# Kernel tuning notes

Hardware: AMD Instinct MI355X
Metric: run time of the kernel (lower is better)

## Reference

```python
import jax, jax.numpy as jnp
import numpy as np

SEQ_LEN = 256
INPUT_DIM = 1
HIDDEN = 2048
CLASSES = 10
BATCH = 128


def setup_inputs() -> dict:
    key = jax.random.key(0)
    ks = jax.random.split(key, 6)
    x = jax.random.normal(ks[0], (BATCH, SEQ_LEN), dtype=jnp.float32)
    # Gate order along the 4H axis: g (cell candidate), i, f, o.
    Wx = jax.random.normal(ks[1], (INPUT_DIM, 4 * HIDDEN), dtype=jnp.float32) * 0.1
    Wh = jax.random.normal(ks[2], (HIDDEN, 4 * HIDDEN), dtype=jnp.float32) * (1.0 / np.sqrt(HIDDEN))
    b = jax.random.normal(ks[3], (4 * HIDDEN,), dtype=jnp.float32) * 0.1
    Wph = jax.random.normal(ks[4], (HIDDEN, CLASSES), dtype=jnp.float32) * (1.0 / np.sqrt(HIDDEN))
    bp = jax.random.normal(ks[5], (CLASSES,), dtype=jnp.float32) * 0.1
    return {"x": x, "Wx": Wx, "Wh": Wh, "b": b, "Wph": Wph, "bp": bp}


def reference(x, Wx, Wh, b, Wph, bp):
    B, T = x.shape
    H = Wh.shape[0]
    # Original loops over seq_length - 1 timesteps.
    xs = x[:, : T - 1].T[:, :, None]  # [T-1, B, 1]

    def step(carry, x_t):
        h, c = carry
        z = x_t @ Wx + h @ Wh + b  # [B, 4H] fused gate GEMM
        g = jnp.tanh(z[:, 0 * H:1 * H])
        i = jax.nn.sigmoid(z[:, 1 * H:2 * H])
        f = jax.nn.sigmoid(z[:, 2 * H:3 * H])
        o = jax.nn.sigmoid(z[:, 3 * H:4 * H])
        c = g * i + c * f
        h = jnp.tanh(c) * o
        return (h, c), None

    h0 = jnp.zeros((B, H), dtype=x.dtype)
    c0 = jnp.zeros((B, H), dtype=x.dtype)
    (h, _), _ = jax.lax.scan(step, (h0, c0), xs)
    logits = h @ Wph + bp
    return jax.nn.softmax(logits, axis=1)
```

## Files before the change

kernel.cpp:

```cpp
#include <hip/hip_runtime.h>
#include <hip/hip_bf16.h>

#define SEQ_LEN 256
#define HIDDEN  2048
#define CLASSES 10
#define BATCH   128
#define NWG     256
#define WG_THREADS 512
#define STEPS   (SEQ_LEN - 1)
#define KTILES  64
#define LDS_WH  131072
#define LDS_ALL (LDS_WH + 4096)

typedef __attribute__((ext_vector_type(8))) short  bf16x8;
typedef __attribute__((ext_vector_type(8))) unsigned short u16x8;
typedef __attribute__((ext_vector_type(4))) float  f32x4;
typedef __attribute__((ext_vector_type(4))) unsigned int u32x4;

#define WHP_OFF  0
#define HB_OFF   33554432UL
#define HF_OFF   (HB_OFF + 4UL * 524288UL)
#define BAR_OFF  (HF_OFF + 1048576UL)

__device__ __forceinline__ unsigned short f2bf(float f) {
    unsigned int u = __float_as_uint(f);
    return (unsigned short)((u + 0x7FFFu + ((u >> 16) & 1u)) >> 16);
}
__device__ __forceinline__ float sigm(float z)  { return 1.0f / (1.0f + __expf(-z)); }
__device__ __forceinline__ float tanh_f(float z){ return 2.0f / (1.0f + __expf(-2.0f * z)) - 1.0f; }

__device__ __forceinline__ unsigned int aload(const unsigned int* p) {
    return __hip_atomic_load(p, __ATOMIC_RELAXED, __HIP_MEMORY_SCOPE_AGENT);
}
__device__ __forceinline__ void astore(unsigned int* p, unsigned int v) {
    __hip_atomic_store(p, v, __ATOMIC_RELAXED, __HIP_MEMORY_SCOPE_AGENT);
}

__global__ void lstm_pack_kernel(const float* __restrict__ Wh,
                                 unsigned short* __restrict__ whp,
                                 unsigned short* __restrict__ hbufs,
                                 unsigned int* __restrict__ bar) {
    int chunk = blockIdx.x * 256 + threadIdx.x;
    int lane = chunk & 63;
    int nt   = (chunk >> 6) & 1;
    int kt   = (chunk >> 7) & 63;
    int W    = chunk >> 13;
    int q = lane >> 4, l16 = lane & 15;
    int c32  = nt * 16 + l16;
    int gate = c32 >> 3, u = c32 & 7;
    int n    = gate * 2048 + W * 8 + u;
    int k0   = kt * 32 + q * 8;
    u16x8 frag;
    #pragma unroll
    for (int j = 0; j < 8; ++j)
        frag[j] = f2bf(Wh[(size_t)(k0 + j) * 8192 + n]);
    ((u16x8*)whp)[chunk] = frag;

    if (chunk < 32768) ((u32x4*)hbufs)[chunk] = (u32x4){0, 0, 0, 0};
    if (chunk < 2048) bar[chunk] = 0u;
}

__device__ __forceinline__ void grid_barrier(unsigned int* bar, unsigned int phase,
                                             bool do_inv, int W) {
    __syncthreads();
    if (threadIdx.x < 64) {
        const int lane = threadIdx.x;
        if (lane == 0) astore(&bar[W], phase);
        if (W < 8) {
            unsigned int* sl = &bar[W * 32 + (lane & 31)];
            while (!__all((int)(aload(sl) >= phase)))
                __builtin_amdgcn_s_sleep(1);
            if (lane == 0) astore(&bar[512 + 16 * W], phase);
            if (W == 0) {
                unsigned int* dn = &bar[512 + 16 * (lane & 7)];
                while (!__all((int)(aload(dn) >= phase)))
                    __builtin_amdgcn_s_sleep(1);
                if (lane < 32) astore(&bar[1024 + 16 * lane], phase);
            }
        }
        if (lane == 0 && W != 0) {
            unsigned int* rl = &bar[1024 + 16 * (W & 31)];
            while (aload(rl) < phase)
                __builtin_amdgcn_s_sleep(1);
        }
        if (do_inv)
            __builtin_amdgcn_fence(__ATOMIC_ACQUIRE, "agent");
    }
    __syncthreads();
}

__global__ __launch_bounds__(WG_THREADS, 2) void lstm_persist(
    const float* __restrict__ x,  const float* __restrict__ Wx,
    const float* __restrict__ b,  const float* __restrict__ Wph,
    const float* __restrict__ bp, const unsigned short* __restrict__ whp,
    unsigned short* hbufs, float* hfin,
    unsigned int* bar, float* out)
{
    extern __shared__ char lds[];
    const int tid = threadIdx.x;
    const int W   = blockIdx.x;

    {
        const u32x4* src = (const u32x4*)whp + (size_t)W * 8192;
        u32x4* dst = (u32x4*)lds;
        for (int i = tid; i < 8192; i += WG_THREADS) dst[i] = src[i];
    }
    unsigned short* hstage = (unsigned short*)(lds + LDS_WH);
    __syncthreads();

    const int lane = tid & 63;
    const int wv   = tid >> 6;
    const int q    = lane >> 4;
    const int l16  = lane & 15;
    const int s    = (lane >> 3) & 1;
    const int u    = lane & 7;
    const int rowA = wv * 16 + l16;
    const int row0 = wv * 16 + q * 4;
    const int colh = W * 8 + u;

    const int n0 = ((l16) >> 3) * 2048 + W * 8 + (l16 & 7);
    const int n1 = ((16 + l16) >> 3) * 2048 + W * 8 + ((16 + l16) & 7);
    const float wx0 = Wx[n0], bb0 = b[n0];
    const float wx1 = Wx[n1], bb1 = b[n1];

    const int abase = q * 128 + rowA;

    float c_state[4] = {0.f, 0.f, 0.f, 0.f};

    for (int t = 0; t < STEPS; ++t) {
        unsigned short* hcur  = hbufs + (size_t)(t & 3) * 262144;
        unsigned short* hnext = hbufs + (size_t)((t + 1) & 3) * 262144;

        const bf16x8* hc8 = (const bf16x8*)hcur;
        const char* lp = lds + lane * 16;

        float xv[4];
        #pragma unroll
        for (int r = 0; r < 4; ++r) xv[r] = x[(row0 + r) * SEQ_LEN + t];

        f32x4 acc0 = {0.f, 0.f, 0.f, 0.f};
        f32x4 acc1 = {0.f, 0.f, 0.f, 0.f};
        bf16x8 a_cur = hc8[abase];
        #pragma unroll 8
        for (int kt = 0; kt < KTILES; ++kt) {
            bf16x8 a_nxt = (kt < KTILES - 1) ? hc8[abase + (kt + 1) * 512] : a_cur;
            bf16x8 b0 = *(const bf16x8*)(lp + (kt * 2 + 0) * 1024);
            bf16x8 b1 = *(const bf16x8*)(lp + (kt * 2 + 1) * 1024);
            acc0 = __builtin_amdgcn_mfma_f32_16x16x32_bf16(a_cur, b0, acc0, 0, 0, 0);
            acc1 = __builtin_amdgcn_mfma_f32_16x16x32_bf16(a_cur, b1, acc1, 0, 0, 0);
            a_cur = a_nxt;
        }

        const bool last = (t == STEPS - 1);
        #pragma unroll
        for (int r = 0; r < 4; ++r) {
            float z0 = acc0[r] + xv[r] * wx0 + bb0;
            float z1 = acc1[r] + xv[r] * wx1 + bb1;
            float p0 = __shfl_xor(z0, 8, 64);
            float p1 = __shfl_xor(z1, 8, 64);
            float zg = s ? p0 : z0;
            float zi = s ? z0 : p0;
            float zf = s ? p1 : z1;
            float zo = s ? z1 : p1;
            float cn = tanh_f(zg) * sigm(zi) + c_state[r] * sigm(zf);
            c_state[r] = cn;
            float h = tanh_f(cn) * sigm(zo);
            if (s == 0) {
                hstage[(row0 + r) * 8 + u] = f2bf(h);
                if (last)
                    __hip_atomic_store(&hfin[(row0 + r) * HIDDEN + colh], h,
                                       __ATOMIC_RELAXED, __HIP_MEMORY_SCOPE_AGENT);
            }
        }
        __syncthreads();
        astore(&((unsigned int*)hnext)[W * 512 + tid],
               ((const unsigned int*)hstage)[tid]);
        grid_barrier(bar, (unsigned int)(t + 1), (t & 3) == 2 || last, W);
    }

    if (W < BATCH) {
        float part[CLASSES];
        #pragma unroll
        for (int c = 0; c < CLASSES; ++c) part[c] = 0.f;
        for (int k = tid; k < HIDDEN; k += WG_THREADS) {
            float hv = hfin[W * HIDDEN + k];
            #pragma unroll
            for (int c = 0; c < CLASSES; ++c) part[c] += hv * Wph[k * CLASSES + c];
        }
        #pragma unroll
        for (int c = 0; c < CLASSES; ++c)
            for (int off = 32; off > 0; off >>= 1)
                part[c] += __shfl_xor(part[c], off, 64);
        float* red = (float*)(lds + LDS_WH);
        __syncthreads();
        if (lane == 0)
            for (int c = 0; c < CLASSES; ++c) red[wv * CLASSES + c] = part[c];
        __syncthreads();
        if (tid == 0) {
            float lg[CLASSES];
            for (int c = 0; c < CLASSES; ++c) {
                float sm = bp[c];
                for (int w8 = 0; w8 < 8; ++w8) sm += red[w8 * CLASSES + c];
                lg[c] = sm;
            }
            float mx = lg[0];
            for (int c = 1; c < CLASSES; ++c) mx = fmaxf(mx, lg[c]);
            float se = 0.f;
            for (int c = 0; c < CLASSES; ++c) { lg[c] = __expf(lg[c] - mx); se += lg[c]; }
            float inv = 1.0f / se;
            for (int c = 0; c < CLASSES; ++c) out[W * CLASSES + c] = lg[c] * inv;
        }
    }
}

extern "C" void kernel_launch(void* const* d_in, const int* in_sizes, int n_in,
                              void* d_out, int out_size, void* d_ws, size_t ws_size,
                              hipStream_t stream) {
    const float* x   = (const float*)d_in[0];
    const float* Wx  = (const float*)d_in[1];
    const float* Wh  = (const float*)d_in[2];
    const float* b   = (const float*)d_in[3];
    const float* Wph = (const float*)d_in[4];
    const float* bp  = (const float*)d_in[5];
    float* out = (float*)d_out;

    char* ws = (char*)d_ws;
    unsigned short* whp  = (unsigned short*)(ws + WHP_OFF);
    unsigned short* hbufs= (unsigned short*)(ws + HB_OFF);
    float*          hfin = (float*)(ws + HF_OFF);
    unsigned int*   bar  = (unsigned int*)(ws + BAR_OFF);

    hipFuncSetAttribute((const void*)lstm_persist,
                        hipFuncAttributeMaxDynamicSharedMemorySize, LDS_ALL);

    lstm_pack_kernel<<<8192, 256, 0, stream>>>(Wh, whp, hbufs, bar);
    lstm_persist<<<NWG, WG_THREADS, LDS_ALL, stream>>>(x, Wx, b, Wph, bp,
                                                       whp, hbufs, hfin, bar, out);
}
```

Measured before the change: 2.647 ms.

## Flatten grid barrier, deepen h prefetch ring, drop per-step block sync

The grid barrier's third tier is removed: every workgroup now polls the 8 second-level flags directly, and s_sleep is dropped from the spin loops. The A-operand (h) loads from global memory become an 8-deep register ring instead of single-step prefetch, so more loads are in flight during the MFMA chain. Each wave now writes its own slice of the h staging buffer and publishes it itself, which removes one __syncthreads per timestep and halves the LDS staging area. The trade-offs are higher memory polling contention from all 256 workgroups spinning without sleep, and more register pressure from the ring.

```diff
diff --git a/kernel.cpp b/kernel.cpp
--- a/kernel.cpp
+++ b/kernel.cpp
@@ -10,7 +10,7 @@
 #define STEPS   (SEQ_LEN - 1)
 #define KTILES  64
 #define LDS_WH  131072
-#define LDS_ALL (LDS_WH + 4096)
+#define LDS_ALL (LDS_WH + 2048)
 
 typedef __attribute__((ext_vector_type(8))) short  bf16x8;
 typedef __attribute__((ext_vector_type(8))) unsigned short u16x8;
@@ -68,21 +68,11 @@
         if (lane == 0) astore(&bar[W], phase);
         if (W < 8) {
             unsigned int* sl = &bar[W * 32 + (lane & 31)];
-            while (!__all((int)(aload(sl) >= phase)))
-                __builtin_amdgcn_s_sleep(1);
+            while (!__all((int)(aload(sl) >= phase))) { }
             if (lane == 0) astore(&bar[512 + 16 * W], phase);
-            if (W == 0) {
-                unsigned int* dn = &bar[512 + 16 * (lane & 7)];
-                while (!__all((int)(aload(dn) >= phase)))
-                    __builtin_amdgcn_s_sleep(1);
-                if (lane < 32) astore(&bar[1024 + 16 * lane], phase);
-            }
-        }
-        if (lane == 0 && W != 0) {
-            unsigned int* rl = &bar[1024 + 16 * (W & 31)];
-            while (aload(rl) < phase)
-                __builtin_amdgcn_s_sleep(1);
-        }
+        }
+        const unsigned int* dn = &bar[512 + 16 * (lane & 7)];
+        while (!__all((int)(aload(dn) >= phase))) { }
         if (do_inv)
             __builtin_amdgcn_fence(__ATOMIC_ACQUIRE, "agent");
     }
@@ -105,7 +95,6 @@
         u32x4* dst = (u32x4*)lds;
         for (int i = tid; i < 8192; i += WG_THREADS) dst[i] = src[i];
     }
-    unsigned short* hstage = (unsigned short*)(lds + LDS_WH);
     __syncthreads();
 
     const int lane = tid & 63;
@@ -118,6 +107,9 @@
     const int row0 = wv * 16 + q * 4;
     const int colh = W * 8 + u;
 
+    unsigned short* hw  = (unsigned short*)(lds + LDS_WH) + wv * 128;
+    const unsigned int* hwd = (const unsigned int*)(lds + LDS_WH) + wv * 64;
+
     const int n0 = ((l16) >> 3) * 2048 + W * 8 + (l16 & 7);
     const int n1 = ((16 + l16) >> 3) * 2048 + W * 8 + ((16 + l16) & 7);
     const float wx0 = Wx[n0], bb0 = b[n0];
@@ -138,17 +130,20 @@
         #pragma unroll
         for (int r = 0; r < 4; ++r) xv[r] = x[(row0 + r) * SEQ_LEN + t];
 
+        bf16x8 ring[8];
+        #pragma unroll
+        for (int j = 0; j < 8; ++j) ring[j] = hc8[abase + j * 512];
+
         f32x4 acc0 = {0.f, 0.f, 0.f, 0.f};
         f32x4 acc1 = {0.f, 0.f, 0.f, 0.f};
-        bf16x8 a_cur = hc8[abase];
         #pragma unroll 8
         for (int kt = 0; kt < KTILES; ++kt) {
-            bf16x8 a_nxt = (kt < KTILES - 1) ? hc8[abase + (kt + 1) * 512] : a_cur;
+            bf16x8 a = ring[kt & 7];
+            if (kt + 8 < KTILES) ring[kt & 7] = hc8[abase + (kt + 8) * 512];
             bf16x8 b0 = *(const bf16x8*)(lp + (kt * 2 + 0) * 1024);
             bf16x8 b1 = *(const bf16x8*)(lp + (kt * 2 + 1) * 1024);
-            acc0 = __builtin_amdgcn_mfma_f32_16x16x32_bf16(a_cur, b0, acc0, 0, 0, 0);
-            acc1 = __builtin_amdgcn_mfma_f32_16x16x32_bf16(a_cur, b1, acc1, 0, 0, 0);
-            a_cur = a_nxt;
+            acc0 = __builtin_amdgcn_mfma_f32_16x16x32_bf16(a, b0, acc0, 0, 0, 0);
+            acc1 = __builtin_amdgcn_mfma_f32_16x16x32_bf16(a, b1, acc1, 0, 0, 0);
         }
 
         const bool last = (t == STEPS - 1);
@@ -166,15 +161,14 @@
             c_state[r] = cn;
             float h = tanh_f(cn) * sigm(zo);
             if (s == 0) {
-                hstage[(row0 + r) * 8 + u] = f2bf(h);
+                hw[(q * 4 + r) * 8 + u] = f2bf(h);
                 if (last)
                     __hip_atomic_store(&hfin[(row0 + r) * HIDDEN + colh], h,
                                        __ATOMIC_RELAXED, __HIP_MEMORY_SCOPE_AGENT);
             }
         }
-        __syncthreads();
-        astore(&((unsigned int*)hnext)[W * 512 + tid],
-               ((const unsigned int*)hstage)[tid]);
+        astore(&((unsigned int*)hnext)[W * 512 + wv * 64 + lane], hwd[lane]);
+
         grid_barrier(bar, (unsigned int)(t + 1), (t & 3) == 2 || last, W);
     }
 
```

Result: slower. 3.057 ms (+15.5%).
